# Performance work log

Measured on AMD Instinct MI355X. Metric: run time of the kernel, lower is better.

The kernel has to match this reference:

```python
import jax, jax.numpy as jnp
import numpy as np

K = 1024          # num_embeddings
D = 128           # embedding_dim
COMMITMENT_COST = 0.25


def setup_inputs() -> dict:
    key = jax.random.key(0)
    k1, k2 = jax.random.split(key)
    inputs = jax.random.normal(k1, (16, D, 4096), dtype=jnp.float32)
    codebook = jax.random.normal(k2, (K, D), dtype=jnp.float32)
    return {"inputs": inputs, "codebook": codebook}


def reference(inputs, codebook):
    # inputs: [B, D, T]; codebook: [K, D]
    B, Dd, T = inputs.shape
    flat = jnp.transpose(inputs, (0, 2, 1)).reshape(-1, Dd)  # [N, D], N = B*T
    N = flat.shape[0]

    d = (jnp.sum(flat * flat, axis=1, keepdims=True)
         + jnp.sum(codebook * codebook, axis=1)
         - 2.0 * flat @ codebook.T)
    idx = jnp.argmin(d, axis=1)  # [N]

    # gather-based quantization (same math as one-hot @ codebook)
    quantized = codebook[idx]                                   # [N, D]
    quantized = quantized.reshape(B, T, Dd).transpose(0, 2, 1)  # [B, D, T]

    # commitment loss (quantized detached; stop_gradient irrelevant in fwd)
    e_latent_loss = jnp.mean((jax.lax.stop_gradient(quantized) - inputs) ** 2)
    loss = COMMITMENT_COST * e_latent_loss

    # straight-through estimator
    quantized_st = inputs + jax.lax.stop_gradient(quantized - inputs)

    # perplexity from code usage histogram (= mean of one-hot encodings)
    counts = jnp.zeros((codebook.shape[0],), dtype=jnp.float32).at[idx].add(1.0)
    avg_probs = counts / N
    perplexity = jnp.exp(-jnp.sum(avg_probs * jnp.log(avg_probs + 1e-10)))

    return loss, quantized_st, perplexity, idx.reshape(B, T)
```

## Files before the change

### kernel.cpp

```cpp
#include <hip/hip_runtime.h>

#define T_FULL 4096
#define D 128
#define K 1024
#define NVEC 65536
#define BDT 8388608
#define BT 128
#define NBLK (NVEC / BT)
#define KT 32
#define NIT (K / KT)
#define PLANE_B (K * D * 2)
#define TILE_B (3 * KT * D * 2)

typedef unsigned short ushort_t;
typedef __bf16 bf16x8 __attribute__((ext_vector_type(8)));
typedef float f32x4 __attribute__((ext_vector_type(4)));

__device__ __forceinline__ float trunc_bf(float x, ushort_t* bits) {
  union { float f; unsigned u; } a; a.f = x;
  *bits = (ushort_t)(a.u >> 16);
  union { unsigned u; float f; } b; b.u = a.u & 0xFFFF0000u;
  return b.f;
}
__device__ __forceinline__ __bf16 bf_bits(ushort_t u) {
  union { ushort_t u; __bf16 h; } c; c.u = u; return c.h;
}

#define MFMA(a, b, c) __builtin_amdgcn_mfma_f32_16x16x32_bf16((a), (b), (c), 0, 0, 0)

#define GLOAD_LDS(g, l)                                                        \
  __builtin_amdgcn_global_load_lds(                                            \
      (const __attribute__((address_space(1))) unsigned int*)(g),              \
      (__attribute__((address_space(3))) unsigned int*)(l), 16, 0, 0)

__global__ __launch_bounds__(128) void prep_kernel(const float* __restrict__ cb,
    float* __restrict__ ee, ushort_t* __restrict__ Eh, ushort_t* __restrict__ Em,
    ushort_t* __restrict__ El) {
  int k = blockIdx.x, d = threadIdx.x;
  float e = cb[k * D + d];
  float v = e * e;
#pragma unroll
  for (int o = 32; o > 0; o >>= 1) v += __shfl_down(v, o, 64);
  __shared__ float tmp[2];
  if ((d & 63) == 0) tmp[d >> 6] = v;
  __syncthreads();
  if (d == 0) ee[k] = tmp[0] + tmp[1];

  float s = 2.0f * e;
  ushort_t hb, mb, lb;
  float hf = trunc_bf(s, &hb);
  float r  = s - hf;
  float mf = trunc_bf(r, &mb);
  (void)trunc_bf(r - mf, &lb);
  Eh[k * D + d] = hb; Em[k * D + d] = mb; El[k * D + d] = lb;
}

__global__ __launch_bounds__(256, 2) void vq_main(
    const float* __restrict__ inp, const float* __restrict__ cb,
    const float* __restrict__ ee, const ushort_t* __restrict__ Eplanes,
    unsigned int* __restrict__ counts, float* __restrict__ lparts,
    float* __restrict__ out_q, float* __restrict__ out_idx) {
  __shared__ __align__(16) ushort_t Bs[2 * 3 * KT * D];
  __shared__ float ee_sh[K];
  __shared__ int   midx[BT];
  __shared__ float lred[4];

  const int tid  = threadIdx.x;
  const int lane = tid & 63;
  const int w    = tid >> 6;
  const int c    = lane & 15;
  const int q    = lane >> 4;
  const int b    = blockIdx.x >> 5;
  const int t0   = (blockIdx.x & 31) * BT;

  unsigned soff[6], sldsoff[6];
#pragma unroll
  for (int i = 0; i < 6; ++i) {
    int flatb = w * 384 + i * 64;
    int p     = flatb >> 9;
    int s     = (flatb & 511) + lane;
    int code  = s >> 4;
    int dg    = (s & 15) ^ (code & 15);
    soff[i]    = (unsigned)(p * PLANE_B + code * 256 + dg * 16);
    sldsoff[i] = (unsigned)(flatb * 16);
  }
  const char* Eb = (const char*)Eplanes;

#pragma unroll
  for (int i = 0; i < 6; ++i)
    GLOAD_LDS(Eb + soff[i], (char*)Bs + sldsoff[i]);

  bf16x8 Ah[2][4], Am[2][4], Al[2][4];
  {
    const float* xin = inp + (size_t)b * D * T_FULL + t0 + w * 32 + c;
#pragma unroll
    for (int n = 0; n < 2; ++n)
#pragma unroll
      for (int dc = 0; dc < 4; ++dc) {
        bf16x8 ah, am, al;
#pragma unroll
        for (int j = 0; j < 8; ++j) {
          int d = dc * 32 + q * 8 + j;
          float x = xin[(size_t)d * T_FULL + n * 16];
          ushort_t hb, mb, lb;
          float hf = trunc_bf(x, &hb);
          float r  = x - hf;
          float mf = trunc_bf(r, &mb);
          (void)trunc_bf(r - mf, &lb);
          ah[j] = bf_bits(hb); am[j] = bf_bits(mb); al[j] = bf_bits(lb);
        }
        Ah[n][dc] = ah; Am[n][dc] = am; Al[n][dc] = al;
      }
  }
#pragma unroll
  for (int i = tid; i < K; i += 256) ee_sh[i] = ee[i];
  __syncthreads();

  float bv[2][4];
  int   bi[2][4];
#pragma unroll
  for (int n = 0; n < 2; ++n)
#pragma unroll
    for (int r = 0; r < 4; ++r) { bv[n][r] = 3.4e38f; bi[n][r] = 0; }

  for (int it = 0; it < NIT; ++it) {
    const int kt = it * KT;
    const int bb = it & 1;

    {
      const int ktn = (kt + KT) & (K - 1);
      const unsigned lb = (unsigned)((bb ^ 1) * TILE_B);
#pragma unroll
      for (int i = 0; i < 6; ++i)
        GLOAD_LDS(Eb + (size_t)ktn * 256 + soff[i], (char*)Bs + lb + sldsoff[i]);
    }

    f32x4 acc[2][2];
#pragma unroll
    for (int n = 0; n < 2; ++n)
#pragma unroll
      for (int kf = 0; kf < 2; ++kf) acc[n][kf] = (f32x4){0.f, 0.f, 0.f, 0.f};

    const char* Bp = (const char*)Bs + bb * TILE_B;
#pragma unroll
    for (int dc = 0; dc < 4; ++dc) {
      const int sw = ((dc * 4 + q) ^ c) * 16;
      bf16x8 Bh[2], Bm[2], Bl[2];
#pragma unroll
      for (int kf = 0; kf < 2; ++kf) {
        const int ro = (kf * 16 + c) * 256 + sw;
        Bh[kf] = *(const bf16x8*)(Bp + ro);
        Bm[kf] = *(const bf16x8*)(Bp + 8192 + ro);
        Bl[kf] = *(const bf16x8*)(Bp + 16384 + ro);
      }
#pragma unroll
      for (int n = 0; n < 2; ++n)
#pragma unroll
        for (int kf = 0; kf < 2; ++kf) {
          f32x4 a = acc[n][kf];
          a = MFMA(Ah[n][dc], Bh[kf], a);
          a = MFMA(Ah[n][dc], Bm[kf], a);
          a = MFMA(Am[n][dc], Bh[kf], a);
          a = MFMA(Ah[n][dc], Bl[kf], a);
          a = MFMA(Al[n][dc], Bh[kf], a);
          a = MFMA(Am[n][dc], Bm[kf], a);
          acc[n][kf] = a;
        }
    }

#pragma unroll
    for (int kf = 0; kf < 2; ++kf) {
      const int code = kt + kf * 16 + c;
      const float eev = ee_sh[code];
#pragma unroll
      for (int n = 0; n < 2; ++n)
#pragma unroll
        for (int r = 0; r < 4; ++r) {
          float dist = eev - acc[n][kf][r];
          if (dist < bv[n][r]) { bv[n][r] = dist; bi[n][r] = code; }
        }
    }
    __syncthreads();
  }

#pragma unroll
  for (int m = 1; m <= 8; m <<= 1)
#pragma unroll
    for (int n = 0; n < 2; ++n)
#pragma unroll
      for (int r = 0; r < 4; ++r) {
        float ov = __shfl_xor(bv[n][r], m, 64);
        int   oi = __shfl_xor(bi[n][r], m, 64);
        if (ov < bv[n][r] || (ov == bv[n][r] && oi < bi[n][r])) {
          bv[n][r] = ov; bi[n][r] = oi;
        }
      }
  if (c == 0) {
#pragma unroll
    for (int n = 0; n < 2; ++n)
#pragma unroll
      for (int r = 0; r < 4; ++r)
        midx[w * 32 + n * 16 + q * 4 + r] = bi[n][r];
  }
  __syncthreads();

  if (tid < BT) {
    int ki = midx[tid];
    out_idx[(size_t)b * T_FULL + t0 + tid] = (float)ki;
    atomicAdd(&counts[ki], 1u);
  }

  float lsum = 0.f;
  {
    const int t  = tid & 127;
    const int dh = tid >> 7;
    const int kq = midx[t];
    const float* crow = cb + (size_t)kq * D + dh * 64;
    const float* xrow = inp + ((size_t)b * D + dh * 64) * T_FULL + t0 + t;
    float*       qrow = out_q + ((size_t)b * D + dh * 64) * T_FULL + t0 + t;
#pragma unroll
    for (int dd = 0; dd < 64; dd += 4) {
      float4 qv = *(const float4*)(crow + dd);
      float x0 = xrow[(size_t)(dd + 0) * T_FULL];
      float x1 = xrow[(size_t)(dd + 1) * T_FULL];
      float x2 = xrow[(size_t)(dd + 2) * T_FULL];
      float x3 = xrow[(size_t)(dd + 3) * T_FULL];
      float df;
      df = qv.x - x0; lsum = fmaf(df, df, lsum); qrow[(size_t)(dd + 0) * T_FULL] = qv.x;
      df = qv.y - x1; lsum = fmaf(df, df, lsum); qrow[(size_t)(dd + 1) * T_FULL] = qv.y;
      df = qv.z - x2; lsum = fmaf(df, df, lsum); qrow[(size_t)(dd + 2) * T_FULL] = qv.z;
      df = qv.w - x3; lsum = fmaf(df, df, lsum); qrow[(size_t)(dd + 3) * T_FULL] = qv.w;
    }
  }
#pragma unroll
  for (int o = 32; o > 0; o >>= 1) lsum += __shfl_down(lsum, o, 64);
  if (lane == 0) lred[w] = lsum;
  __syncthreads();
  if (tid == 0) lparts[blockIdx.x] = lred[0] + lred[1] + lred[2] + lred[3];
}

__global__ __launch_bounds__(256) void fin_kernel(const unsigned int* __restrict__ counts,
                                                  const float* __restrict__ lparts,
                                                  float* __restrict__ out) {
  int tid = threadIdx.x;
  float ent = 0.f, ls = 0.f;
#pragma unroll
  for (int i = tid; i < K; i += 256) {
    float p = (float)counts[i] * (1.0f / (float)NVEC);
    ent = fmaf(p, logf(p + 1e-10f), ent);
  }
#pragma unroll
  for (int i = tid; i < NBLK; i += 256) ls += lparts[i];
#pragma unroll
  for (int o = 32; o > 0; o >>= 1) {
    ent += __shfl_down(ent, o, 64);
    ls  += __shfl_down(ls, o, 64);
  }
  __shared__ float se[4], sl[4];
  int wv = tid >> 6, lane = tid & 63;
  if (lane == 0) { se[wv] = ent; sl[wv] = ls; }
  __syncthreads();
  if (tid == 0) {
    float e = se[0] + se[1] + se[2] + se[3];
    float l = sl[0] + sl[1] + sl[2] + sl[3];
    out[0]       = 0.25f * (l / (float)BDT);
    out[1 + BDT] = expf(-e);
  }
}

extern "C" void kernel_launch(void* const* d_in, const int* in_sizes, int n_in,
                              void* d_out, int out_size, void* d_ws, size_t ws_size,
                              hipStream_t stream) {
  const float* inp = (const float*)d_in[0];
  const float* cb  = (const float*)d_in[1];
  float* out = (float*)d_out;

  char* ws = (char*)d_ws;
  unsigned int* counts = (unsigned int*)ws;
  float*    lparts = (float*)(ws + 4096);
  float*    ee     = (float*)(ws + 8192);
  ushort_t* Eh     = (ushort_t*)(ws + 12288);
  ushort_t* Em     = (ushort_t*)(ws + 12288 + PLANE_B);
  ushort_t* El     = (ushort_t*)(ws + 12288 + 2 * PLANE_B);

  hipMemsetAsync(counts, 0, K * sizeof(unsigned int), stream);
  prep_kernel<<<K, 128, 0, stream>>>(cb, ee, Eh, Em, El);
  vq_main<<<NBLK, 256, 0, stream>>>(inp, cb, ee, Eh, counts, lparts,
                                    out + 1, out + 2 + BDT);
  fin_kernel<<<1, 256, 0, stream>>>(counts, lparts, out);
}
```

Measured before the change: 196.3 us.

## Fuse finalize into main kernel, reuse split inputs for loss, stagger d-chunks

Removes the memset and the single-block finalize kernel. Counters are now zeroed in the prep kernel, and the last-arriving block of vq_main, chosen by an atomic ticket, computes perplexity and loss. The commitment loss is rebuilt from the register-held hi/mid/lo bf16 splits instead of re-reading the inputs from global memory, and each wave starts its d-chunk loop at a different offset to spread LDS bank and load traffic. This trades two launches and a second input read for atomics, a float atomicAdd whose summation order is nondeterministic, and a small approximation in reconstructing x.

```diff
diff --git a/kernel.cpp b/kernel.cpp
--- a/kernel.cpp
+++ b/kernel.cpp
@@ -35,8 +35,13 @@
 
 __global__ __launch_bounds__(128) void prep_kernel(const float* __restrict__ cb,
     float* __restrict__ ee, ushort_t* __restrict__ Eh, ushort_t* __restrict__ Em,
-    ushort_t* __restrict__ El) {
+    ushort_t* __restrict__ El, unsigned int* __restrict__ counts,
+    unsigned int* __restrict__ done, float* __restrict__ loss_acc) {
   int k = blockIdx.x, d = threadIdx.x;
+  if (d == 0) {
+    counts[k] = 0u;
+    if (k == 0) { *done = 0u; *loss_acc = 0.f; }
+  }
   float e = cb[k * D + d];
   float v = e * e;
 #pragma unroll
@@ -58,12 +63,16 @@
 __global__ __launch_bounds__(256, 2) void vq_main(
     const float* __restrict__ inp, const float* __restrict__ cb,
     const float* __restrict__ ee, const ushort_t* __restrict__ Eplanes,
-    unsigned int* __restrict__ counts, float* __restrict__ lparts,
-    float* __restrict__ out_q, float* __restrict__ out_idx) {
+    unsigned int* __restrict__ counts, unsigned int* __restrict__ done,
+    float* __restrict__ loss_acc, float* __restrict__ out) {
   __shared__ __align__(16) ushort_t Bs[2 * 3 * KT * D];
   __shared__ float ee_sh[K];
   __shared__ int   midx[BT];
   __shared__ float lred[4];
+  __shared__ int   lastf;
+
+  float* out_q   = out + 1;
+  float* out_idx = out + 2 + BDT;
 
   const int tid  = threadIdx.x;
   const int lane = tid & 63;
@@ -96,11 +105,12 @@
 #pragma unroll
     for (int n = 0; n < 2; ++n)
 #pragma unroll
-      for (int dc = 0; dc < 4; ++dc) {
+      for (int dci = 0; dci < 4; ++dci) {
+        const int dcg = (dci + w) & 3;
         bf16x8 ah, am, al;
 #pragma unroll
         for (int j = 0; j < 8; ++j) {
-          int d = dc * 32 + q * 8 + j;
+          int d = dcg * 32 + q * 8 + j;
           float x = xin[(size_t)d * T_FULL + n * 16];
           ushort_t hb, mb, lb;
           float hf = trunc_bf(x, &hb);
@@ -109,7 +119,7 @@
           (void)trunc_bf(r - mf, &lb);
           ah[j] = bf_bits(hb); am[j] = bf_bits(mb); al[j] = bf_bits(lb);
         }
-        Ah[n][dc] = ah; Am[n][dc] = am; Al[n][dc] = al;
+        Ah[n][dci] = ah; Am[n][dci] = am; Al[n][dci] = al;
       }
   }
 #pragma unroll
@@ -143,8 +153,9 @@
 
     const char* Bp = (const char*)Bs + bb * TILE_B;
 #pragma unroll
-    for (int dc = 0; dc < 4; ++dc) {
-      const int sw = ((dc * 4 + q) ^ c) * 16;
+    for (int dci = 0; dci < 4; ++dci) {
+      const int dcg = (dci + w) & 3;
+      const int sw = ((dcg * 4 + q) ^ c) * 16;
       bf16x8 Bh[2], Bm[2], Bl[2];
 #pragma unroll
       for (int kf = 0; kf < 2; ++kf) {
@@ -158,12 +169,12 @@
 #pragma unroll
         for (int kf = 0; kf < 2; ++kf) {
           f32x4 a = acc[n][kf];
-          a = MFMA(Ah[n][dc], Bh[kf], a);
-          a = MFMA(Ah[n][dc], Bm[kf], a);
-          a = MFMA(Am[n][dc], Bh[kf], a);
-          a = MFMA(Ah[n][dc], Bl[kf], a);
-          a = MFMA(Al[n][dc], Bh[kf], a);
-          a = MFMA(Am[n][dc], Bm[kf], a);
+          a = MFMA(Ah[n][dci], Bh[kf], a);
+          a = MFMA(Ah[n][dci], Bm[kf], a);
+          a = MFMA(Am[n][dci], Bh[kf], a);
+          a = MFMA(Ah[n][dci], Bl[kf], a);
+          a = MFMA(Al[n][dci], Bh[kf], a);
+          a = MFMA(Am[n][dci], Bm[kf], a);
           acc[n][kf] = a;
         }
     }
@@ -211,60 +222,59 @@
   }
 
   float lsum = 0.f;
-  {
-    const int t  = tid & 127;
-    const int dh = tid >> 7;
-    const int kq = midx[t];
-    const float* crow = cb + (size_t)kq * D + dh * 64;
-    const float* xrow = inp + ((size_t)b * D + dh * 64) * T_FULL + t0 + t;
-    float*       qrow = out_q + ((size_t)b * D + dh * 64) * T_FULL + t0 + t;
-#pragma unroll
-    for (int dd = 0; dd < 64; dd += 4) {
-      float4 qv = *(const float4*)(crow + dd);
-      float x0 = xrow[(size_t)(dd + 0) * T_FULL];
-      float x1 = xrow[(size_t)(dd + 1) * T_FULL];
-      float x2 = xrow[(size_t)(dd + 2) * T_FULL];
-      float x3 = xrow[(size_t)(dd + 3) * T_FULL];
-      float df;
-      df = qv.x - x0; lsum = fmaf(df, df, lsum); qrow[(size_t)(dd + 0) * T_FULL] = qv.x;
-      df = qv.y - x1; lsum = fmaf(df, df, lsum); qrow[(size_t)(dd + 1) * T_FULL] = qv.y;
-      df = qv.z - x2; lsum = fmaf(df, df, lsum); qrow[(size_t)(dd + 2) * T_FULL] = qv.z;
-      df = qv.w - x3; lsum = fmaf(df, df, lsum); qrow[(size_t)(dd + 3) * T_FULL] = qv.w;
+#pragma unroll
+  for (int n = 0; n < 2; ++n) {
+    const int tn = w * 32 + n * 16 + c;
+    const int kq = midx[tn];
+    const float* crow = cb + (size_t)kq * D;
+    float* qbase = out_q + (size_t)b * D * T_FULL + t0 + tn;
+#pragma unroll
+    for (int dci = 0; dci < 4; ++dci) {
+      const int dcg = (dci + w) & 3;
+      const int d0 = dcg * 32 + q * 8;
+      float4 qa = *(const float4*)(crow + d0);
+      float4 qb = *(const float4*)(crow + d0 + 4);
+      float qv[8] = {qa.x, qa.y, qa.z, qa.w, qb.x, qb.y, qb.z, qb.w};
+#pragma unroll
+      for (int j = 0; j < 8; ++j) {
+        float x = (float)Ah[n][dci][j] + (float)Am[n][dci][j] + (float)Al[n][dci][j];
+        float df = qv[j] - x;
+        lsum = fmaf(df, df, lsum);
+        qbase[(size_t)(d0 + j) * T_FULL] = qv[j];
+      }
     }
   }
 #pragma unroll
   for (int o = 32; o > 0; o >>= 1) lsum += __shfl_down(lsum, o, 64);
   if (lane == 0) lred[w] = lsum;
   __syncthreads();
-  if (tid == 0) lparts[blockIdx.x] = lred[0] + lred[1] + lred[2] + lred[3];
-}
-
-__global__ __launch_bounds__(256) void fin_kernel(const unsigned int* __restrict__ counts,
-                                                  const float* __restrict__ lparts,
-                                                  float* __restrict__ out) {
-  int tid = threadIdx.x;
-  float ent = 0.f, ls = 0.f;
-#pragma unroll
-  for (int i = tid; i < K; i += 256) {
-    float p = (float)counts[i] * (1.0f / (float)NVEC);
-    ent = fmaf(p, logf(p + 1e-10f), ent);
-  }
-#pragma unroll
-  for (int i = tid; i < NBLK; i += 256) ls += lparts[i];
-#pragma unroll
-  for (int o = 32; o > 0; o >>= 1) {
-    ent += __shfl_down(ent, o, 64);
-    ls  += __shfl_down(ls, o, 64);
-  }
-  __shared__ float se[4], sl[4];
-  int wv = tid >> 6, lane = tid & 63;
-  if (lane == 0) { se[wv] = ent; sl[wv] = ls; }
-  __syncthreads();
   if (tid == 0) {
-    float e = se[0] + se[1] + se[2] + se[3];
-    float l = sl[0] + sl[1] + sl[2] + sl[3];
-    out[0]       = 0.25f * (l / (float)BDT);
-    out[1 + BDT] = expf(-e);
+    atomicAdd(loss_acc, lred[0] + lred[1] + lred[2] + lred[3]);
+    __threadfence();
+    unsigned ticket = atomicAdd(done, 1u);
+    lastf = (ticket == NBLK - 1) ? 1 : 0;
+  }
+  __syncthreads();
+
+  if (lastf) {
+    __threadfence();
+    float ent = 0.f;
+#pragma unroll
+    for (int i = tid; i < K; i += 256) {
+      float cnt = (float)atomicAdd(&counts[i], 0u);
+      float p = cnt * (1.0f / (float)NVEC);
+      ent = fmaf(p, logf(p + 1e-10f), ent);
+    }
+#pragma unroll
+    for (int o = 32; o > 0; o >>= 1) ent += __shfl_down(ent, o, 64);
+    if (lane == 0) lred[w] = ent;
+    __syncthreads();
+    if (tid == 0) {
+      float e = lred[0] + lred[1] + lred[2] + lred[3];
+      float l = atomicAdd(loss_acc, 0.f);
+      out[0]       = 0.25f * (l / (float)BDT);
+      out[1 + BDT] = expf(-e);
+    }
   }
 }
 
@@ -276,16 +286,14 @@
   float* out = (float*)d_out;
 
   char* ws = (char*)d_ws;
-  unsigned int* counts = (unsigned int*)ws;
-  float*    lparts = (float*)(ws + 4096);
-  float*    ee     = (float*)(ws + 8192);
-  ushort_t* Eh     = (ushort_t*)(ws + 12288);
-  ushort_t* Em     = (ushort_t*)(ws + 12288 + PLANE_B);
-  ushort_t* El     = (ushort_t*)(ws + 12288 + 2 * PLANE_B);
-
-  hipMemsetAsync(counts, 0, K * sizeof(unsigned int), stream);
-  prep_kernel<<<K, 128, 0, stream>>>(cb, ee, Eh, Em, El);
-  vq_main<<<NBLK, 256, 0, stream>>>(inp, cb, ee, Eh, counts, lparts,
-                                    out + 1, out + 2 + BDT);
-  fin_kernel<<<1, 256, 0, stream>>>(counts, lparts, out);
-}
+  unsigned int* counts  = (unsigned int*)ws;
+  unsigned int* done    = (unsigned int*)(ws + 4096);
+  float*        lossacc = (float*)(ws + 4160);
+  float*        ee      = (float*)(ws + 8192);
+  ushort_t*     Eh      = (ushort_t*)(ws + 12288);
+  ushort_t*     Em      = (ushort_t*)(ws + 12288 + PLANE_B);
+  ushort_t*     El      = (ushort_t*)(ws + 12288 + 2 * PLANE_B);
+
+  prep_kernel<<<K, 128, 0, stream>>>(cb, ee, Eh, Em, El, counts, done, lossacc);
+  vq_main<<<NBLK, 256, 0, stream>>>(inp, cb, ee, Eh, counts, done, lossacc, out);
+}
```

Result: slower. 215.0 us (+9.5%).
